# Performance work log

Hardware: AMD Instinct MI355X
Metric: run time of the kernel (lower is better)

The kernel has to match this reference:

```python
import jax, jax.numpy as jnp
import numpy as np

B, N, C = 8, 4096, 1024
ATT_DIM = 512
M = 64  # num_outputs


def setup_inputs() -> dict:
    key = jax.random.key(0)
    k_x, k_w, k_b, k_av = jax.random.split(key, 4)
    x = jax.random.normal(k_x, (B, N, C), dtype=jnp.float32)
    # nn.Linear(input_dim, attention_dim): weight (att, C), bias (att,)
    lim = 1.0 / np.sqrt(C)
    W = jax.random.uniform(k_w, (ATT_DIM, C), dtype=jnp.float32, minval=-lim, maxval=lim)
    b = jax.random.uniform(k_b, (ATT_DIM,), dtype=jnp.float32, minval=-lim, maxval=lim)
    # torch.rand -> uniform [0,1)
    attention_vectors = jax.random.uniform(k_av, (M, ATT_DIM), dtype=jnp.float32)
    return {"x": x, "W": W, "b": b, "attention_vectors": attention_vectors}


def reference(x, W, b, attention_vectors):
    # linear projection: (B,N,C) @ (C,att) + bias -> (B,N,att)
    scores = jnp.einsum('bnc,dc->bnd', x, W) + b
    # learned-query attention logits: (B,M,N)
    logits = jnp.einsum('bnd,md->bmn', scores, attention_vectors)
    weights = jax.nn.softmax(logits, axis=-1)
    # pool original features: (B,M,N) @ (B,N,C) -> (B,M,C)
    return jnp.einsum('bmn,bnc->bmc', weights, x)
```

## Files before the change

### kernel.cpp

```cpp
#include <hip/hip_runtime.h>
#include <hip/hip_bf16.h>

#define Bn 8
#define Nn 4096
#define Cn 1024
#define Dn 512
#define Mn 64

typedef __hip_bfloat16 bf16;
typedef __attribute__((ext_vector_type(8))) short short8;
typedef __attribute__((ext_vector_type(4))) float f32x4;

#define MFMA16(a, b, c) __builtin_amdgcn_mfma_f32_16x16x32_bf16((a), (b), (c), 0, 0, 0)

__device__ inline short bfbits(float f) {
  union { bf16 b; short s; } u;
  u.b = __float2bfloat16(f);
  return u.s;
}

__global__ __launch_bounds__(256) void prep_kernel(
    const float* __restrict__ W, const float* __restrict__ bias,
    const float* __restrict__ av, bf16* __restrict__ Vhi,
    bf16* __restrict__ Vlo, float* __restrict__ c0) {
  const int m = blockIdx.x;
  const int c = blockIdx.y * 256 + threadIdx.x;
  float acc = 0.f;
  for (int d = 0; d < Dn; ++d) {
    acc = fmaf(av[m * Dn + d], W[d * Cn + c], acc);
  }
  const bf16 hi = __float2bfloat16(acc);
  Vhi[m * Cn + c] = hi;
  Vlo[m * Cn + c] = __float2bfloat16(acc - __bfloat162float(hi));

  if (blockIdx.y == 0) {
    __shared__ float red[256];
    const int t = threadIdx.x;
    red[t] = av[m * Dn + t] * bias[t] + av[m * Dn + t + 256] * bias[t + 256];
    __syncthreads();
    for (int off = 128; off > 0; off >>= 1) {
      if (t < off) red[t] += red[t + off];
      __syncthreads();
    }
    if (t == 0) c0[m] = red[0];
  }
}

__global__ __launch_bounds__(256) void logits_kernel(
    const float* __restrict__ x, const bf16* __restrict__ Vhi,
    const bf16* __restrict__ Vlo, const float* __restrict__ c0,
    float* __restrict__ logits) {
  const int n0 = blockIdx.x * 64;
  const int b = blockIdx.y;
  const int t = threadIdx.x;
  __shared__ short Xs[64][72];
  __shared__ short Vs[64][72];
  const int w = t >> 6, lane = t & 63, lr = lane & 15, q = lane >> 4;
  f32x4 acc[4];
#pragma unroll
  for (int i = 0; i < 4; ++i) acc[i] = (f32x4){0.f, 0.f, 0.f, 0.f};

  const int r = t >> 2;
  const int cseg = (t & 3) * 16;
  const float* xrow = x + (size_t)(b * Nn + n0 + r) * Cn;

  for (int kc = 0; kc < Cn; kc += 64) {
    {
      const float4 f0 = *(const float4*)(xrow + kc + cseg);
      const float4 f1 = *(const float4*)(xrow + kc + cseg + 4);
      const float4 f2 = *(const float4*)(xrow + kc + cseg + 8);
      const float4 f3 = *(const float4*)(xrow + kc + cseg + 12);
      short8 s0, s1;
      s0[0] = bfbits(f0.x); s0[1] = bfbits(f0.y); s0[2] = bfbits(f0.z); s0[3] = bfbits(f0.w);
      s0[4] = bfbits(f1.x); s0[5] = bfbits(f1.y); s0[6] = bfbits(f1.z); s0[7] = bfbits(f1.w);
      s1[0] = bfbits(f2.x); s1[1] = bfbits(f2.y); s1[2] = bfbits(f2.z); s1[3] = bfbits(f2.w);
      s1[4] = bfbits(f3.x); s1[5] = bfbits(f3.y); s1[6] = bfbits(f3.z); s1[7] = bfbits(f3.w);
      *(short8*)&Xs[r][cseg] = s0;
      *(short8*)&Xs[r][cseg + 8] = s1;
      *(float4*)&Vs[r][cseg]     = *(const float4*)(Vhi + r * Cn + kc + cseg);
      *(float4*)&Vs[r][cseg + 8] = *(const float4*)(Vhi + r * Cn + kc + cseg + 8);
    }
    __syncthreads();
#pragma unroll
    for (int kk = 0; kk < 64; kk += 32) {
      const short8 a = *(const short8*)&Xs[w * 16 + lr][kk + q * 8];
#pragma unroll
      for (int mt = 0; mt < 4; ++mt) {
        const short8 bh = *(const short8*)&Vs[mt * 16 + lr][kk + q * 8];
        acc[mt] = MFMA16(a, bh, acc[mt]);
        const short8 bl = *(const short8*)(Vlo + (size_t)(mt * 16 + lr) * Cn + kc + kk + q * 8);
        acc[mt] = MFMA16(a, bl, acc[mt]);
      }
    }
    __syncthreads();
  }
#pragma unroll
  for (int mt = 0; mt < 4; ++mt) {
    const int m = mt * 16 + lr;
    const float bb = c0[m];
    float4 o;
    o.x = acc[mt][0] + bb; o.y = acc[mt][1] + bb;
    o.z = acc[mt][2] + bb; o.w = acc[mt][3] + bb;
    *(float4*)&logits[(size_t)(b * Mn + m) * Nn + n0 + w * 16 + q * 4] = o;
  }
}

__global__ __launch_bounds__(256) void softmax_kernel(
    const float* __restrict__ logits, bf16* __restrict__ wgt) {
  const int row = blockIdx.x;
  const int t = threadIdx.x;
  const float* L = logits + (size_t)row * Nn;
  float v[16];
  float mx = -3.4e38f;
#pragma unroll
  for (int i = 0; i < 16; ++i) {
    v[i] = L[t + 256 * i];
    mx = fmaxf(mx, v[i]);
  }
#pragma unroll
  for (int off = 32; off > 0; off >>= 1) mx = fmaxf(mx, __shfl_down(mx, off));
  __shared__ float sred[4];
  if ((t & 63) == 0) sred[t >> 6] = mx;
  __syncthreads();
  mx = fmaxf(fmaxf(sred[0], sred[1]), fmaxf(sred[2], sred[3]));
  float sum = 0.f;
#pragma unroll
  for (int i = 0; i < 16; ++i) {
    v[i] = __expf(v[i] - mx);
    sum += v[i];
  }
#pragma unroll
  for (int off = 32; off > 0; off >>= 1) sum += __shfl_down(sum, off);
  __syncthreads();
  if ((t & 63) == 0) sred[t >> 6] = sum;
  __syncthreads();
  const float inv = 1.f / (sred[0] + sred[1] + sred[2] + sred[3]);
#pragma unroll
  for (int i = 0; i < 16; ++i)
    wgt[(size_t)row * Nn + t + 256 * i] = __float2bfloat16(v[i] * inv);
}

__global__ __launch_bounds__(256) void pool_kernel(
    const float* __restrict__ x, const bf16* __restrict__ wgt,
    float* __restrict__ part) {
  const int cbase = blockIdx.x * 64;
  const int b = blockIdx.y;
  const int ks = blockIdx.z;
  const int t = threadIdx.x;
  __shared__ short XT[64][72];
  const int w = t >> 6, lane = t & 63, lr = lane & 15, q = lane >> 4;
  const int mh = (w & 1) * 32, ch = (w >> 1) * 32;
  f32x4 acc[2][2];
#pragma unroll
  for (int i = 0; i < 2; ++i)
#pragma unroll
    for (int j = 0; j < 2; ++j) acc[i][j] = (f32x4){0.f, 0.f, 0.f, 0.f};

  const int kr = t >> 2;
  const int cs = (t & 3) * 16;
  const float* xb = x + (size_t)b * Nn * Cn;
  const bf16* wrow0 = wgt + (size_t)(b * Mn + mh + lr) * Nn;
  const bf16* wrow1 = wgt + (size_t)(b * Mn + mh + 16 + lr) * Nn;

  for (int kc = 0; kc < Nn / 2; kc += 64) {
    const int kglob = ks * (Nn / 2) + kc;
    {
      const float* src = xb + (size_t)(kglob + kr) * Cn + cbase + cs;
      const float4 f0 = *(const float4*)(src);
      const float4 f1 = *(const float4*)(src + 4);
      const float4 f2 = *(const float4*)(src + 8);
      const float4 f3 = *(const float4*)(src + 12);
      XT[cs +  0][kr] = bfbits(f0.x); XT[cs +  1][kr] = bfbits(f0.y);
      XT[cs +  2][kr] = bfbits(f0.z); XT[cs +  3][kr] = bfbits(f0.w);
      XT[cs +  4][kr] = bfbits(f1.x); XT[cs +  5][kr] = bfbits(f1.y);
      XT[cs +  6][kr] = bfbits(f1.z); XT[cs +  7][kr] = bfbits(f1.w);
      XT[cs +  8][kr] = bfbits(f2.x); XT[cs +  9][kr] = bfbits(f2.y);
      XT[cs + 10][kr] = bfbits(f2.z); XT[cs + 11][kr] = bfbits(f2.w);
      XT[cs + 12][kr] = bfbits(f3.x); XT[cs + 13][kr] = bfbits(f3.y);
      XT[cs + 14][kr] = bfbits(f3.z); XT[cs + 15][kr] = bfbits(f3.w);
    }
    __syncthreads();
#pragma unroll
    for (int kk = 0; kk < 64; kk += 32) {
      const short8 a0 = *(const short8*)(wrow0 + kglob + kk + q * 8);
      const short8 a1 = *(const short8*)(wrow1 + kglob + kk + q * 8);
      const short8 b0 = *(const short8*)&XT[ch + lr][kk + q * 8];
      const short8 b1 = *(const short8*)&XT[ch + 16 + lr][kk + q * 8];
      acc[0][0] = MFMA16(a0, b0, acc[0][0]);
      acc[0][1] = MFMA16(a0, b1, acc[0][1]);
      acc[1][0] = MFMA16(a1, b0, acc[1][0]);
      acc[1][1] = MFMA16(a1, b1, acc[1][1]);
    }
    __syncthreads();
  }
  float* pout = part + (size_t)(ks * Bn + b) * Mn * Cn;
#pragma unroll
  for (int mi = 0; mi < 2; ++mi)
#pragma unroll
    for (int ci = 0; ci < 2; ++ci) {
      const int m = mh + mi * 16 + q * 4;
      const int c = cbase + ch + ci * 16 + lr;
#pragma unroll
      for (int reg = 0; reg < 4; ++reg)
        pout[(size_t)(m + reg) * Cn + c] = acc[mi][ci][reg];
    }
}

__global__ __launch_bounds__(256) void reduce_kernel(
    const float* __restrict__ part, float* __restrict__ out) {
  const int idx = blockIdx.x * 256 + threadIdx.x;
  out[idx] = part[idx] + part[idx + Bn * Mn * Cn];
}

extern "C" void kernel_launch(void* const* d_in, const int* in_sizes, int n_in,
                              void* d_out, int out_size, void* d_ws, size_t ws_size,
                              hipStream_t stream) {
  const float* x = (const float*)d_in[0];
  const float* W = (const float*)d_in[1];
  const float* bias = (const float*)d_in[2];
  const float* av = (const float*)d_in[3];
  float* out = (float*)d_out;
  char* ws = (char*)d_ws;

  bf16* Vhi = (bf16*)(ws + 0);
  bf16* Vlo = (bf16*)(ws + 131072);
  float* c0 = (float*)(ws + 262144);
  float* logits = (float*)(ws + 263168);
  bf16* wgt = (bf16*)(ws + 8651776);
  float* part = (float*)(ws + 12846080);

  prep_kernel<<<dim3(Mn, Cn / 256), 256, 0, stream>>>(W, bias, av, Vhi, Vlo, c0);
  logits_kernel<<<dim3(Nn / 64, Bn), 256, 0, stream>>>(x, Vhi, Vlo, c0, logits);
  softmax_kernel<<<Bn * Mn, 256, 0, stream>>>(logits, wgt);
  pool_kernel<<<dim3(Cn / 64, Bn, 2), 256, 0, stream>>>(x, wgt, part);
  reduce_kernel<<<(Bn * Mn * Cn) / 256, 256, 0, stream>>>(part, out);
}
```

Baseline: 299.5 us.

## Split prep reduction, drop LDS in logits, vectorize pool transpose, 4-way split-K

The prep kernel now splits the D-reduction across four wave groups with unrolled independent accumulators and a shared-memory combine, which gives more blocks and more ILP. The logits kernel drops LDS staging and barriers: each lane loads its x fragment straight from global with one-step register prefetch and reads Vhi/Vlo directly. The pool kernel transposes x into LDS with vectorized 4x4 short stores instead of scalar stores, and split-K goes from 2 to 4, with a float4 reduce over the four partials. The costs are more partial-buffer traffic and Vhi/Vlo fragments that are no longer shared between waves, so they depend on the cache.

```diff
diff --git a/kernel.cpp b/kernel.cpp
--- a/kernel.cpp
+++ b/kernel.cpp
@@ -9,6 +9,7 @@
 
 typedef __hip_bfloat16 bf16;
 typedef __attribute__((ext_vector_type(8))) short short8;
+typedef __attribute__((ext_vector_type(4))) short short4x;
 typedef __attribute__((ext_vector_type(4))) float f32x4;
 
 #define MFMA16(a, b, c) __builtin_amdgcn_mfma_f32_16x16x32_bf16((a), (b), (c), 0, 0, 0)
@@ -24,25 +25,38 @@
     const float* __restrict__ av, bf16* __restrict__ Vhi,
     bf16* __restrict__ Vlo, float* __restrict__ c0) {
   const int m = blockIdx.x;
-  const int c = blockIdx.y * 256 + threadIdx.x;
-  float acc = 0.f;
-  for (int d = 0; d < Dn; ++d) {
-    acc = fmaf(av[m * Dn + d], W[d * Cn + c], acc);
-  }
-  const bf16 hi = __float2bfloat16(acc);
-  Vhi[m * Cn + c] = hi;
-  Vlo[m * Cn + c] = __float2bfloat16(acc - __bfloat162float(hi));
-
+  const int t = threadIdx.x;
+  const int cl = t & 63, dg = t >> 6;
+  const int c = blockIdx.y * 64 + cl;
+  const float* wp = W + (size_t)(dg * 128) * Cn + c;
+  const float* ap = av + m * Dn + dg * 128;
+  float a0 = 0.f, a1 = 0.f, a2 = 0.f, a3 = 0.f;
+#pragma unroll 8
+  for (int i = 0; i < 128; i += 4) {
+    a0 = fmaf(ap[i + 0], wp[(size_t)(i + 0) * Cn], a0);
+    a1 = fmaf(ap[i + 1], wp[(size_t)(i + 1) * Cn], a1);
+    a2 = fmaf(ap[i + 2], wp[(size_t)(i + 2) * Cn], a2);
+    a3 = fmaf(ap[i + 3], wp[(size_t)(i + 3) * Cn], a3);
+  }
+  __shared__ float red[256];
+  red[t] = (a0 + a1) + (a2 + a3);
+  __syncthreads();
+  const float v = red[cl] + red[cl + 64] + red[cl + 128] + red[cl + 192];
+  if (dg == 0) {
+    const bf16 hi = __float2bfloat16(v);
+    Vhi[m * Cn + c] = hi;
+    Vlo[m * Cn + c] = __float2bfloat16(v - __bfloat162float(hi));
+  }
   if (blockIdx.y == 0) {
-    __shared__ float red[256];
-    const int t = threadIdx.x;
+    __syncthreads();
     red[t] = av[m * Dn + t] * bias[t] + av[m * Dn + t + 256] * bias[t + 256];
     __syncthreads();
-    for (int off = 128; off > 0; off >>= 1) {
-      if (t < off) red[t] += red[t + off];
-      __syncthreads();
-    }
-    if (t == 0) c0[m] = red[0];
+    if (t < 64) {
+      float s = red[t] + red[t + 64] + red[t + 128] + red[t + 192];
+#pragma unroll
+      for (int off = 32; off > 0; off >>= 1) s += __shfl_down(s, off);
+      if (t == 0) c0[m] = s;
+    }
   }
 }
 
@@ -53,46 +67,31 @@
   const int n0 = blockIdx.x * 64;
   const int b = blockIdx.y;
   const int t = threadIdx.x;
-  __shared__ short Xs[64][72];
-  __shared__ short Vs[64][72];
   const int w = t >> 6, lane = t & 63, lr = lane & 15, q = lane >> 4;
+  const float* xrow = x + (size_t)(b * Nn + n0 + w * 16 + lr) * Cn + q * 8;
   f32x4 acc[4];
 #pragma unroll
   for (int i = 0; i < 4; ++i) acc[i] = (f32x4){0.f, 0.f, 0.f, 0.f};
 
-  const int r = t >> 2;
-  const int cseg = (t & 3) * 16;
-  const float* xrow = x + (size_t)(b * Nn + n0 + r) * Cn;
-
-  for (int kc = 0; kc < Cn; kc += 64) {
-    {
-      const float4 f0 = *(const float4*)(xrow + kc + cseg);
-      const float4 f1 = *(const float4*)(xrow + kc + cseg + 4);
-      const float4 f2 = *(const float4*)(xrow + kc + cseg + 8);
-      const float4 f3 = *(const float4*)(xrow + kc + cseg + 12);
-      short8 s0, s1;
-      s0[0] = bfbits(f0.x); s0[1] = bfbits(f0.y); s0[2] = bfbits(f0.z); s0[3] = bfbits(f0.w);
-      s0[4] = bfbits(f1.x); s0[5] = bfbits(f1.y); s0[6] = bfbits(f1.z); s0[7] = bfbits(f1.w);
-      s1[0] = bfbits(f2.x); s1[1] = bfbits(f2.y); s1[2] = bfbits(f2.z); s1[3] = bfbits(f2.w);
-      s1[4] = bfbits(f3.x); s1[5] = bfbits(f3.y); s1[6] = bfbits(f3.z); s1[7] = bfbits(f3.w);
-      *(short8*)&Xs[r][cseg] = s0;
-      *(short8*)&Xs[r][cseg + 8] = s1;
-      *(float4*)&Vs[r][cseg]     = *(const float4*)(Vhi + r * Cn + kc + cseg);
-      *(float4*)&Vs[r][cseg + 8] = *(const float4*)(Vhi + r * Cn + kc + cseg + 8);
-    }
-    __syncthreads();
-#pragma unroll
-    for (int kk = 0; kk < 64; kk += 32) {
-      const short8 a = *(const short8*)&Xs[w * 16 + lr][kk + q * 8];
-#pragma unroll
-      for (int mt = 0; mt < 4; ++mt) {
-        const short8 bh = *(const short8*)&Vs[mt * 16 + lr][kk + q * 8];
-        acc[mt] = MFMA16(a, bh, acc[mt]);
-        const short8 bl = *(const short8*)(Vlo + (size_t)(mt * 16 + lr) * Cn + kc + kk + q * 8);
-        acc[mt] = MFMA16(a, bl, acc[mt]);
-      }
-    }
-    __syncthreads();
+  float4 f0 = *(const float4*)(xrow);
+  float4 f1 = *(const float4*)(xrow + 4);
+  for (int k0 = 0; k0 < Cn; k0 += 32) {
+    const float4 c0v = f0, c1v = f1;
+    if (k0 + 32 < Cn) {
+      f0 = *(const float4*)(xrow + k0 + 32);
+      f1 = *(const float4*)(xrow + k0 + 36);
+    }
+    short8 a;
+    a[0] = bfbits(c0v.x); a[1] = bfbits(c0v.y); a[2] = bfbits(c0v.z); a[3] = bfbits(c0v.w);
+    a[4] = bfbits(c1v.x); a[5] = bfbits(c1v.y); a[6] = bfbits(c1v.z); a[7] = bfbits(c1v.w);
+    const int ka = k0 + q * 8;
+#pragma unroll
+    for (int mt = 0; mt < 4; ++mt) {
+      const short8 bh = *(const short8*)(Vhi + (size_t)(mt * 16 + lr) * Cn + ka);
+      acc[mt] = MFMA16(a, bh, acc[mt]);
+      const short8 bl = *(const short8*)(Vlo + (size_t)(mt * 16 + lr) * Cn + ka);
+      acc[mt] = MFMA16(a, bl, acc[mt]);
+    }
   }
 #pragma unroll
   for (int mt = 0; mt < 4; ++mt) {
@@ -156,28 +155,29 @@
 #pragma unroll
     for (int j = 0; j < 2; ++j) acc[i][j] = (f32x4){0.f, 0.f, 0.f, 0.f};
 
-  const int kr = t >> 2;
-  const int cs = (t & 3) * 16;
+  const int g = t & 15;
+  const int h = t >> 4;
   const float* xb = x + (size_t)b * Nn * Cn;
   const bf16* wrow0 = wgt + (size_t)(b * Mn + mh + lr) * Nn;
   const bf16* wrow1 = wgt + (size_t)(b * Mn + mh + 16 + lr) * Nn;
 
-  for (int kc = 0; kc < Nn / 2; kc += 64) {
-    const int kglob = ks * (Nn / 2) + kc;
+  for (int kc = 0; kc < Nn / 4; kc += 64) {
+    const int kglob = ks * (Nn / 4) + kc;
     {
-      const float* src = xb + (size_t)(kglob + kr) * Cn + cbase + cs;
-      const float4 f0 = *(const float4*)(src);
-      const float4 f1 = *(const float4*)(src + 4);
-      const float4 f2 = *(const float4*)(src + 8);
-      const float4 f3 = *(const float4*)(src + 12);
-      XT[cs +  0][kr] = bfbits(f0.x); XT[cs +  1][kr] = bfbits(f0.y);
-      XT[cs +  2][kr] = bfbits(f0.z); XT[cs +  3][kr] = bfbits(f0.w);
-      XT[cs +  4][kr] = bfbits(f1.x); XT[cs +  5][kr] = bfbits(f1.y);
-      XT[cs +  6][kr] = bfbits(f1.z); XT[cs +  7][kr] = bfbits(f1.w);
-      XT[cs +  8][kr] = bfbits(f2.x); XT[cs +  9][kr] = bfbits(f2.y);
-      XT[cs + 10][kr] = bfbits(f2.z); XT[cs + 11][kr] = bfbits(f2.w);
-      XT[cs + 12][kr] = bfbits(f3.x); XT[cs + 13][kr] = bfbits(f3.y);
-      XT[cs + 14][kr] = bfbits(f3.z); XT[cs + 15][kr] = bfbits(f3.w);
+      const float* src = xb + (size_t)(kglob + 4 * g) * Cn + cbase + 4 * h;
+      const float4 r0 = *(const float4*)(src);
+      const float4 r1 = *(const float4*)(src + Cn);
+      const float4 r2 = *(const float4*)(src + 2 * Cn);
+      const float4 r3 = *(const float4*)(src + 3 * Cn);
+      short4x w0, w1, w2, w3;
+      w0[0] = bfbits(r0.x); w0[1] = bfbits(r1.x); w0[2] = bfbits(r2.x); w0[3] = bfbits(r3.x);
+      w1[0] = bfbits(r0.y); w1[1] = bfbits(r1.y); w1[2] = bfbits(r2.y); w1[3] = bfbits(r3.y);
+      w2[0] = bfbits(r0.z); w2[1] = bfbits(r1.z); w2[2] = bfbits(r2.z); w2[3] = bfbits(r3.z);
+      w3[0] = bfbits(r0.w); w3[1] = bfbits(r1.w); w3[2] = bfbits(r2.w); w3[3] = bfbits(r3.w);
+      *(short4x*)&XT[4 * h + 0][4 * g] = w0;
+      *(short4x*)&XT[4 * h + 1][4 * g] = w1;
+      *(short4x*)&XT[4 * h + 2][4 * g] = w2;
+      *(short4x*)&XT[4 * h + 3][4 * g] = w3;
     }
     __syncthreads();
 #pragma unroll
@@ -193,7 +193,7 @@
     }
     __syncthreads();
   }
-  float* pout = part + (size_t)(ks * Bn + b) * Mn * Cn;
+  float* pout = part + ((size_t)ks * Bn + b) * Mn * Cn;
 #pragma unroll
   for (int mi = 0; mi < 2; ++mi)
 #pragma unroll
@@ -208,8 +208,16 @@
 
 __global__ __launch_bounds__(256) void reduce_kernel(
     const float* __restrict__ part, float* __restrict__ out) {
-  const int idx = blockIdx.x * 256 + threadIdx.x;
-  out[idx] = part[idx] + part[idx + Bn * Mn * Cn];
+  const int i = blockIdx.x * 256 + threadIdx.x;
+  const float4* p = (const float4*)part;
+  const int S4 = (Bn * Mn * Cn) / 4;
+  const float4 v0 = p[i], v1 = p[i + S4], v2 = p[i + 2 * S4], v3 = p[i + 3 * S4];
+  float4 o;
+  o.x = (v0.x + v1.x) + (v2.x + v3.x);
+  o.y = (v0.y + v1.y) + (v2.y + v3.y);
+  o.z = (v0.z + v1.z) + (v2.z + v3.z);
+  o.w = (v0.w + v1.w) + (v2.w + v3.w);
+  ((float4*)out)[i] = o;
 }
 
 extern "C" void kernel_launch(void* const* d_in, const int* in_sizes, int n_in,
@@ -229,9 +237,9 @@
   bf16* wgt = (bf16*)(ws + 8651776);
   float* part = (float*)(ws + 12846080);
 
-  prep_kernel<<<dim3(Mn, Cn / 256), 256, 0, stream>>>(W, bias, av, Vhi, Vlo, c0);
+  prep_kernel<<<dim3(Mn, Cn / 64), 256, 0, stream>>>(W, bias, av, Vhi, Vlo, c0);
   logits_kernel<<<dim3(Nn / 64, Bn), 256, 0, stream>>>(x, Vhi, Vlo, c0, logits);
   softmax_kernel<<<Bn * Mn, 256, 0, stream>>>(logits, wgt);
-  pool_kernel<<<dim3(Cn / 64, Bn, 2), 256, 0, stream>>>(x, wgt, part);
-  reduce_kernel<<<(Bn * Mn * Cn) / 256, 256, 0, stream>>>(part, out);
-}
+  pool_kernel<<<dim3(Cn / 64, Bn, 4), 256, 0, stream>>>(x, wgt, part);
+  reduce_kernel<<<(Bn * Mn * Cn) / 1024, 256, 0, stream>>>(part, out);
+}
```

New measurement: 286.8 us. 4.2% less time.
